# Performance work log

Hardware: AMD Instinct MI355X
Metric: run time of the kernel (lower is better)

The kernel has to match this reference:

```python
import jax, jax.numpy as jnp
import numpy as np

STALK_DIM = 8
K = 5
MARGIN = 0.5
TAU = 0.01
EPS_GAP = 1e-4


def _sheaf_eigenvalues(points, W):
    """Eigenvalues of the sheaf Laplacian L = delta^T delta on a point cloud.

    points: (n, d_in), W: (s, d_in) projection weight (nn.Linear, no bias).
    Faithful to the torch loop, but assembles L directly from its s x s blocks
    (L = delta^T delta expanded per edge) instead of materializing dense delta.
    """
    X = points @ W.T                       # (n, s)
    n, s = X.shape

    # --- fixed topology: KNN on detached coordinates (torch no_grad) ---
    Xd = jax.lax.stop_gradient(X)
    d2 = jnp.sum((Xd[:, None, :] - Xd[None, :, :]) ** 2, axis=-1)  # (n, n)
    nn_idx = jnp.argsort(d2, axis=1)[:, 1:K + 1]                    # (n, K), skip self
    A = jnp.zeros((n, n), dtype=bool).at[jnp.arange(n)[:, None], nn_idx].set(True)
    A = A | A.T                                                     # undirected
    triu = jnp.triu(jnp.ones((n, n), dtype=bool), 1)
    M = (A & triu).astype(points.dtype)    # (n, n) edge mask, canonical i < j

    # --- restriction maps for all ordered pairs i < j (mask selects edges) ---
    d = X[None, :, :] - X[:, None, :]      # d[i, j] = X[j] - X[i], (n, n, s)
    dn = jnp.linalg.norm(d, axis=-1) + 1e-12
    dhat = d / dn[..., None]
    alpha = jnp.minimum(dn, 1.0)
    I_s = jnp.eye(s, dtype=points.dtype)
    # R_ij = I - alpha * dhat dhat^T   (n, n, s, s)
    R = I_s - alpha[..., None, None] * (dhat[..., :, None] * dhat[..., None, :])
    RtR = jnp.einsum('ijab,ijac->ijbc', R, R)

    # --- L = delta^T delta, per edge (i<j): row block [.. I .. -R ..]
    #     contributes  L[i,i]+=I,  L[j,j]+=R^T R,  L[i,j]+=-R,  L[j,i]+=-R^T
    Off = -(M[..., None, None] * R)                     # nonzero only for i<j
    Lb = Off + jnp.swapaxes(jnp.swapaxes(Off, 0, 1), 2, 3)  # add lower blocks
    deg = M.sum(axis=1)                                  # I-blocks at node i
    Djj = jnp.einsum('ij,ijab->jab', M, RtR)             # R^T R blocks at node j
    diag = deg[:, None, None] * I_s + Djj                # (n, s, s)
    Lb = Lb.at[jnp.arange(n), jnp.arange(n)].add(diag)
    L = Lb.transpose(0, 2, 1, 3).reshape(n * s, n * s)
    L = 0.5 * (L + L.T)

    eigs = jnp.linalg.eigvalsh(L)          # ascending, (n*s,)
    return jnp.clip(eigs, 0.0)


def _spectral_gap(eigs):
    gates = jax.nn.sigmoid((eigs - EPS_GAP) / TAU)
    return jnp.sum(eigs * gates) / (jnp.sum(gates) + 1e-12)


def setup_inputs() -> dict:
    key = jax.random.key(0)
    kq, kp, kn, kw = jax.random.split(key, 4)
    n_q, n_pn, d_in = 256, 256, 768
    q_emb = jax.random.normal(kq, (n_q, d_in), dtype=jnp.float32)
    pos_emb = jax.random.normal(kp, (n_pn, d_in), dtype=jnp.float32)
    neg_emb = jax.random.normal(kn, (n_pn, d_in), dtype=jnp.float32)
    # orthogonal init for the projection, as in nn.init.orthogonal_
    G = jax.random.normal(kw, (d_in, STALK_DIM), dtype=jnp.float32)
    Q, _ = jnp.linalg.qr(G)                # (d_in, s) with orthonormal columns
    W = Q.T                                # (s, d_in)
    return {"q_emb": q_emb, "pos_emb": pos_emb, "neg_emb": neg_emb, "W": W}


def reference(q_emb, pos_emb, neg_emb, W):
    pos_cloud = jnp.concatenate([q_emb, pos_emb], axis=0)
    neg_cloud = jnp.concatenate([q_emb, neg_emb], axis=0)
    gap_pos = _spectral_gap(_sheaf_eigenvalues(pos_cloud, W))
    gap_neg = _spectral_gap(_sheaf_eigenvalues(neg_cloud, W))
    triplet = jax.nn.relu(gap_pos - gap_neg + MARGIN)
    return triplet + 0.1 * gap_pos
```

## Files before the change

### kernel.cpp

```cpp
#include <hip/hip_runtime.h>
#include <math.h>

#define NLS    4096
#define NNODE  512
#define SDIM   8
#define KNN_K  5
#define MAXNBR 128
#define DIN    768
#define NB     32
#define GMEGA  448

#define AGLD(p)    __hip_atomic_load((p), __ATOMIC_RELAXED, __HIP_MEMORY_SCOPE_AGENT)
#define AGST(p, v) __hip_atomic_store((p), (v), __ATOMIC_RELAXED, __HIP_MEMORY_SCOPE_AGENT)

struct Ptrs {
  float* X;
  int*   nn;
  int*   nbr;
  int*   cnt;
  float* y;
  float* acol;
  float* vtw;
  float* xn2;
  float* darr;
  float* ebuf;
  float* e2;
  float* bounds;
  float* eigs;
  float* Vt;
  float* Wt;
  float* c1;
  float* c2;
  int*   barmem;
  float* A0;
  float* A1;
};

__device__ __forceinline__ float* matA(const Ptrs& p, int cloud) {
  return cloud == 0 ? p.A0 : p.A1;
}

__device__ __forceinline__ void tbar(int* bm, int act, int bid, int& gen,
                                     int& leafbase, int& rootbase, bool fence) {
  __syncthreads();
  if (threadIdx.x == 0) {
    gen += 1;
    int perleaf = act >> 5;
    if (fence) __threadfence();
    else       __builtin_amdgcn_s_waitcnt(0);
    int* leaf = bm + ((bid & 31) << 4);
    int old = __hip_atomic_fetch_add(leaf, 1, __ATOMIC_RELAXED, __HIP_MEMORY_SCOPE_AGENT);
    if (old == leafbase + perleaf - 1) {
      int ro = __hip_atomic_fetch_add(bm + 512, 1, __ATOMIC_RELAXED, __HIP_MEMORY_SCOPE_AGENT);
      if (ro == rootbase + 31) AGST(bm + 768, gen);
    }
    leafbase += perleaf;
    rootbase += 32;
    while (AGLD(bm + 768) < gen) __builtin_amdgcn_s_sleep(16);
    if (fence) __threadfence();
  }
  __syncthreads();
}

__global__ void zero_kernel(float* ptr, long n) {
  long i = (long)blockIdx.x * 256 + threadIdx.x;
  if (i < n) ptr[i] = 0.f;
}

__global__ void proj_kernel(Ptrs p, const float* q, const float* pe,
                            const float* ne, const float* W) {
  int idx = blockIdx.x * 256 + threadIdx.x;
  if (idx >= 2 * NNODE * SDIM) return;
  int cloud = idx >> 12;
  int rem   = idx & 4095;
  int node  = rem >> 3, t = rem & 7;
  const float* src = (node < 256) ? (q + (size_t)node * DIN)
                                  : ((cloud == 0 ? pe : ne) + (size_t)(node - 256) * DIN);
  const float* wr = W + (size_t)t * DIN;
  float acc = 0.f;
  for (int i = 0; i < DIN; ++i) acc += src[i] * wr[i];
  p.X[(cloud * NNODE + node) * SDIM + t] = acc;
}

__global__ void knn_kernel(Ptrs p) {
  int i = blockIdx.x, cloud = blockIdx.z;
  int lane = threadIdx.x;
  __shared__ float d2s[NNODE];
  const float* X = p.X + cloud * NNODE * SDIM;
  float xi[SDIM];
  for (int t = 0; t < SDIM; ++t) xi[t] = X[i * SDIM + t];
  for (int j = lane; j < NNODE; j += 64) {
    float s = 0.f;
    for (int t = 0; t < SDIM; ++t) { float d = xi[t] - X[j * SDIM + t]; s += d * d; }
    d2s[j] = (j == i) ? 3.4e38f : s;
  }
  __syncthreads();
  for (int r = 0; r < KNN_K; ++r) {
    float bv = 3.39e38f; int bi = NNODE;
    for (int j = lane; j < NNODE; j += 64) {
      float val = d2s[j];
      if (val < bv || (val == bv && j < bi)) { bv = val; bi = j; }
    }
    for (int o = 32; o > 0; o >>= 1) {
      float ov = __shfl_down(bv, o); int oi = __shfl_down(bi, o);
      if (ov < bv || (ov == bv && oi < bi)) { bv = ov; bi = oi; }
    }
    if (lane == 0) {
      p.nn[(cloud * NNODE + i) * KNN_K + r] = bi;
      d2s[bi] = 3.4e38f;
    }
    __syncthreads();
  }
}

__global__ void adj_kernel(Ptrs p) {
  int idx = blockIdx.x * 256 + threadIdx.x;
  if (idx >= 2 * NNODE) return;
  int cloud = idx >> 9, i = idx & 511;
  const int* nn = p.nn + cloud * NNODE * KNN_K;
  int c = 0;
  for (int j = 0; j < NNODE; ++j) {
    if (j == i) continue;
    bool e = false;
    for (int r = 0; r < KNN_K; ++r)
      if (nn[i * KNN_K + r] == j || nn[j * KNN_K + r] == i) e = true;
    if (e) { if (c < MAXNBR) p.nbr[(cloud * NNODE + i) * MAXNBR + c] = j; ++c; }
  }
  p.cnt[cloud * NNODE + i] = (c > MAXNBR ? MAXNBR : c);
}

__global__ void assemble_kernel(Ptrs p, int cloud0) {
  int i = blockIdx.x;
  int cloud = cloud0 + blockIdx.z;
  float* A = matA(p, cloud);
  const float* X = p.X + cloud * NNODE * SDIM;
  const int* nbr = p.nbr + (cloud * NNODE + i) * MAXNBR;
  int cnt = p.cnt[cloud * NNODE + i];
  int tid = threadIdx.x;

  for (int idx = tid; idx < SDIM * NLS; idx += 256) {
    int t = idx >> 12;
    int c = idx & 4095;
    A[(size_t)(i * SDIM + t) * NLS + c] = 0.f;
  }
  __shared__ float diag[64];
  __shared__ float xi[SDIM];
  if (tid < SDIM) xi[tid] = X[i * SDIM + tid];
  if (tid < 64)   diag[tid] = 0.f;
  __syncthreads();

  for (int s = 0; s < cnt; ++s) {
    int j = nbr[s];
    float d[SDIM], ss = 0.f;
    for (int t = 0; t < SDIM; ++t) { d[t] = X[j * SDIM + t] - xi[t]; ss += d[t] * d[t]; }
    float dn = sqrtf(ss) + 1e-12f;
    float alpha = dn < 1.f ? dn : 1.f;
    float inv = 1.f / dn;
    if (tid < 64) {
      int t = tid >> 3, t2 = tid & 7;
      float ut = d[t] * inv, ut2 = d[t2] * inv;
      A[(size_t)(i * SDIM + t) * NLS + j * SDIM + t2] =
          alpha * ut * ut2 - (t == t2 ? 1.f : 0.f);
      if (j < i) {
        float beta = 2.f * alpha - alpha * alpha;
        diag[tid] += beta * ut * ut2;
      }
    }
  }
  __syncthreads();
  if (tid < 64) {
    int t = tid >> 3, t2 = tid & 7;
    A[(size_t)(i * SDIM + t) * NLS + i * SDIM + t2] =
        (t == t2 ? (float)cnt : 0.f) - diag[tid];
  }
}

__global__ __launch_bounds__(256, 4) void mega_kernel(Ptrs p, int cloud0) {
  const int cloud = cloud0 + blockIdx.z;
  const int bid = blockIdx.x;
  float* A  = matA(p, cloud);
  float* Vt = p.Vt + (size_t)cloud * NB * NLS;
  float* Wt = p.Wt + (size_t)cloud * NB * NLS;
  float* yv = p.y + (size_t)cloud * NLS;
  float* acol = p.acol + (size_t)cloud * NLS;
  float* c1g = p.c1 + (size_t)cloud * NLS * NB;
  float* c2g = p.c2 + (size_t)cloud * NLS * NB;
  float* xn2g = p.xn2 + (size_t)cloud * NLS;
  int* bm = p.barmem + (size_t)cloud * 2048;
  int gen = 0, leafbase = 0, rootbase = 0;
  const int tid = threadIdx.x, lane = tid & 63, wv = tid >> 6;

  __shared__ __align__(16) union {
    float v[NLS + 4];
    struct { float Vr[NB][64], Wr[NB][64], Vc[NB][64], Wc[NB][64]; } t;
  } sh;
  __shared__ float c1w[4][NB], c2w[4][NB];
  __shared__ float c1s[NB], c2s[NB], vks[NB], wks[NB];
  __shared__ float red4[4];

  for (int k0 = 0; k0 + NB <= NLS - 64; k0 += NB) {
    int act = (NLS - k0) >> 3;
    act = (act + 31) & ~31;
    if (act < 64)    act = 64;
    if (act > GMEGA) act = GMEGA;
    if (bid >= act) return;

    for (int jj = 0; jj < NB; ++jj) {
      const int k = k0 + jj, s = k + 1, m = NLS - s;
      const int vbase = s & ~3, vn = NLS - vbase;

      float tau, scale;
      if (jj == 0) {
        const float* src = A + (size_t)k * NLS;
        float xp = 0.f;
        for (int i = tid; i < vn; i += 256) {
          int c = vbase + i;
          float a = (c < s) ? 0.f : AGLD((float*)&src[c]);
          sh.v[i] = a;
          if (c > s) xp += a * a;
        }
        for (int o = 32; o > 0; o >>= 1) xp += __shfl_down(xp, o);
        if (lane == 0) red4[wv] = xp;
        __syncthreads();
        float xnorm2 = red4[0] + red4[1] + red4[2] + red4[3];
        float alpha = sh.v[s - vbase];
        float beta;
        if (xnorm2 > 0.f) {
          beta  = -copysignf(sqrtf(alpha * alpha + xnorm2), alpha);
          tau   = (beta - alpha) / beta;
          scale = 1.f / (alpha - beta);
        } else { beta = alpha; tau = 0.f; scale = 0.f; }
        if (bid == 0 && tid == 0) {
          p.darr[cloud * NLS + k] = AGLD((float*)&src[k]);
          p.ebuf[cloud * NLS + k] = beta;
        }
        __syncthreads();
        for (int i = tid; i < vn; i += 256) {
          int c = vbase + i;
          sh.v[i] = (c == s) ? 1.f : ((c < s) ? 0.f : sh.v[i] * scale);
        }
        __syncthreads();
      } else {
        float xnorm2 = AGLD(&xn2g[k]);
        float alpha  = AGLD(&acol[s]);
        float beta;
        if (xnorm2 > 0.f) {
          beta  = -copysignf(sqrtf(alpha * alpha + xnorm2), alpha);
          tau   = (beta - alpha) / beta;
          scale = 1.f / (alpha - beta);
        } else { beta = alpha; tau = 0.f; scale = 0.f; }
        if (bid == 0 && tid == 0) {
          p.darr[cloud * NLS + k] = AGLD(&acol[k]);
          p.ebuf[cloud * NLS + k] = beta;
        }
        for (int i = tid; i < vn; i += 256) {
          int c = vbase + i;
          float a = (c < s) ? 0.f : AGLD(&acol[c]);
          sh.v[i] = (c == s) ? 1.f : a * scale;
        }
        __syncthreads();
      }

      const int nwav = act << 2;
      int B = (m + nwav - 1) / nwav;
      B = (B + 1) & ~1;
      const int r0 = s + ((bid << 2) + wv) * B;
      int r1 = r0 + B; if (r1 > NLS) r1 = NLS;
      float vtyloc = 0.f, c1p = 0.f, c2p = 0.f;
      const int l2i = lane - 32;
      for (int r = r0; r < r1; r += 2) {
        const bool two = (r + 1 < r1);
        const float* Ar0 = A + (size_t)r * NLS;
        const float* Ar1 = two ? (Ar0 + NLS) : Ar0;
        float acc0 = 0.f, acc1 = 0.f;
        #pragma unroll 4
        for (int c = vbase + (lane << 2); c < NLS; c += 256) {
          const float4 v4 = *(const float4*)(&sh.v[c - vbase]);
          const float4 a0 = *(const float4*)(Ar0 + c);
          const float4 a1 = *(const float4*)(Ar1 + c);
          acc0 += a0.x * v4.x + a0.y * v4.y + a0.z * v4.z + a0.w * v4.w;
          acc1 += a1.x * v4.x + a1.y * v4.y + a1.z * v4.z + a1.w * v4.w;
        }
        for (int o = 32; o > 0; o >>= 1) {
          acc0 += __shfl_down(acc0, o);
          acc1 += __shfl_down(acc1, o);
        }
        float vr0 = sh.v[r - vbase];
        float vr1 = two ? sh.v[r + 1 - vbase] : 0.f;
        if (lane == 0) {
          AGST(&yv[r], acc0);
          if (two) AGST(&yv[r + 1], acc1);
          vtyloc += vr0 * acc0 + vr1 * acc1;
        }
        if (lane < jj) {
          const float* Wl = Wt + (size_t)lane * NLS;
          c1p += Wl[r] * vr0 + (two ? Wl[r + 1] * vr1 : 0.f);
        }
        if (l2i >= 0 && l2i < jj) {
          const float* Vl = Vt + (size_t)l2i * NLS;
          c2p += Vl[r] * vr0 + (two ? Vl[r + 1] * vr1 : 0.f);
        }
      }
      if (lane == 0) red4[wv] = vtyloc;
      if (lane < 32)      c1w[wv][lane] = (lane < jj) ? c1p : 0.f;
      else                c2w[wv][l2i]  = (l2i  < jj) ? c2p : 0.f;
      __syncthreads();
      if (tid == 0) {
        float t = red4[0] + red4[1] + red4[2] + red4[3];
        if (t != 0.f) atomicAdd(&p.vtw[cloud * NLS + k], t);
      }
      if (tid < jj) {
        float t = c1w[0][tid] + c1w[1][tid] + c1w[2][tid] + c1w[3][tid];
        if (t != 0.f) atomicAdd(&c1g[(size_t)k * NB + tid], t);
      } else if (tid >= 64 && tid < 64 + jj) {
        int j2 = tid - 64;
        float t = c2w[0][j2] + c2w[1][j2] + c2w[2][j2] + c2w[3][j2];
        if (t != 0.f) atomicAdd(&c2g[(size_t)k * NB + j2], t);
      }

      tbar(bm, act, bid, gen, leafbase, rootbase, false);

      if (tid < jj) {
        c1s[tid] = AGLD(&c1g[(size_t)k * NB + tid]);
        c2s[tid] = AGLD(&c2g[(size_t)k * NB + tid]);
        vks[tid] = Vt[(size_t)tid * NLS + s];
        wks[tid] = Wt[(size_t)tid * NLS + s];
      }
      __syncthreads();
      float vty = AGLD(&p.vtw[cloud * NLS + k]);
      float dotc = 0.f, corrs = 0.f;
      for (int j2 = 0; j2 < jj; ++j2) {
        dotc  += c1s[j2] * c2s[j2];
        corrs += vks[j2] * c1s[j2] + wks[j2] * c2s[j2];
      }
      float s2v = tau * (vty - 2.f * dotc);
      float ys  = AGLD(&yv[s]);
      float wfirst = tau * ys - tau * corrs - 0.5f * tau * s2v;
      bool havenext = (jj < NB - 1);
      const float* Arow = A + (size_t)s * NLS;
      float xpart = 0.f;
      for (int r = s + (bid << 8) + tid; r < NLS; r += (act << 8)) {
        float vr = sh.v[r - vbase];
        float yr = AGLD(&yv[r]);
        float corr = 0.f, ac2 = 0.f;
        for (int j2 = 0; j2 < jj; ++j2) {
          float vj = Vt[(size_t)j2 * NLS + r];
          float wj = Wt[(size_t)j2 * NLS + r];
          corr += vj * c1s[j2] + wj * c2s[j2];
          ac2  += vj * wks[j2] + wj * vks[j2];
        }
        float wr = tau * yr - tau * corr - 0.5f * tau * s2v * vr;
        AGST(&Vt[(size_t)jj * NLS + r], vr);
        AGST(&Wt[(size_t)jj * NLS + r], wr);
        if (havenext) {
          float ac = Arow[r] - ac2 - (vr * wfirst + wr);
          AGST(&acol[r], ac);
          if (r >= s + 2) xpart += ac * ac;
        }
      }
      if (havenext) {
        for (int o = 32; o > 0; o >>= 1) xpart += __shfl_down(xpart, o);
        if (lane == 0) red4[wv] = xpart;
        __syncthreads();
        if (tid == 0) {
          float t = red4[0] + red4[1] + red4[2] + red4[3];
          if (t != 0.f) atomicAdd(&xn2g[k + 1], t);
        }
      }

      tbar(bm, act, bid, gen, leafbase, rootbase, false);
    }

    {
      const int base2 = k0 + NB;
      const int nt = (NLS - base2 + 63) >> 6;
      const int ntt = nt * nt;
      for (int it = bid; it < ntt; it += act) {
        int by = it / nt, bx = it - by * nt;
        int r0t = base2 + (by << 6), c0t = base2 + (bx << 6);
        __syncthreads();
        for (int idx = tid; idx < NB * 64; idx += 256) {
          int j4 = idx >> 6, i = idx & 63;
          int r = r0t + i, c = c0t + i;
          sh.t.Vr[j4][i] = (r < NLS) ? Vt[(size_t)j4 * NLS + r] : 0.f;
          sh.t.Wr[j4][i] = (r < NLS) ? Wt[(size_t)j4 * NLS + r] : 0.f;
          sh.t.Vc[j4][i] = (c < NLS) ? Vt[(size_t)j4 * NLS + c] : 0.f;
          sh.t.Wc[j4][i] = (c < NLS) ? Wt[(size_t)j4 * NLS + c] : 0.f;
        }
        __syncthreads();
        int ty = tid >> 4, tx = tid & 15;
        float acc[4][4] = {{0.f}};
        for (int j4 = 0; j4 < NB; ++j4) {
          float vr[4], wr[4], vc[4], wc[4];
          for (int a = 0; a < 4; ++a) {
            vr[a] = sh.t.Vr[j4][ty * 4 + a]; wr[a] = sh.t.Wr[j4][ty * 4 + a];
            vc[a] = sh.t.Vc[j4][tx * 4 + a]; wc[a] = sh.t.Wc[j4][tx * 4 + a];
          }
          for (int a = 0; a < 4; ++a)
            for (int b = 0; b < 4; ++b)
              acc[a][b] += vr[a] * wc[b] + wr[a] * vc[b];
        }
        for (int a = 0; a < 4; ++a) {
          int r = r0t + ty * 4 + a;
          int c = c0t + tx * 4;
          if (r < NLS && c < NLS) {
            float4* pa = (float4*)&A[(size_t)r * NLS + c];
            float4 old = *pa;
            old.x -= acc[a][0]; old.y -= acc[a][1];
            old.z -= acc[a][2]; old.w -= acc[a][3];
            *pa = old;
          }
        }
      }
      tbar(bm, act, bid, gen, leafbase, rootbase, true);
    }
  }
}

__global__ void ktrail_kernel(Ptrs p, int cloud0) {
  int cloud = cloud0 + blockIdx.z;
  float* A = matA(p, cloud);
  const int base = NLS - 64;
  int lane = threadIdx.x;
  __shared__ float B[64][65];
  __shared__ float vv[64], ww[64];
  for (int r = 0; r < 64; ++r)
    B[r][lane] = A[(size_t)(base + r) * NLS + base + lane];
  __syncthreads();
  for (int kl = 0; kl <= 61; ++kl) {
    float val = (lane >= kl + 2) ? B[kl][lane] : 0.f;
    float part = val * val;
    for (int o = 32; o > 0; o >>= 1) part += __shfl_xor(part, o);
    float xnorm2 = part;
    float alpha = B[kl][kl + 1];
    float beta, tau, scale;
    if (xnorm2 > 0.f) {
      beta  = -copysignf(sqrtf(alpha * alpha + xnorm2), alpha);
      tau   = (beta - alpha) / beta;
      scale = 1.f / (alpha - beta);
    } else { beta = alpha; tau = 0.f; scale = 0.f; }
    if (lane == 0) {
      p.darr[cloud * NLS + base + kl] = B[kl][kl];
      p.ebuf[cloud * NLS + base + kl] = beta;
    }
    vv[lane] = (lane == kl + 1) ? 1.f : ((lane >= kl + 2) ? B[kl][lane] * scale : 0.f);
    __syncthreads();
    float yv = 0.f;
    if (lane >= kl + 1)
      for (int c = kl + 1; c < 64; ++c) yv += B[lane][c] * vv[c];
    float vy = (lane >= kl + 1) ? vv[lane] * yv : 0.f;
    for (int o = 32; o > 0; o >>= 1) vy += __shfl_xor(vy, o);
    float w = tau * yv - 0.5f * tau * (tau * vy) * vv[lane];
    ww[lane] = (lane >= kl + 1) ? w : 0.f;
    __syncthreads();
    if (lane >= kl + 1) {
      float vr = vv[lane], wr = ww[lane];
      for (int c = kl + 1; c < 64; ++c)
        B[lane][c] -= vr * ww[c] + wr * vv[c];
    }
    __syncthreads();
  }
  if (lane == 0) {
    p.darr[cloud * NLS + base + 62] = B[62][62];
    p.darr[cloud * NLS + base + 63] = B[63][63];
    p.ebuf[cloud * NLS + base + 62] = B[63][62];
    p.ebuf[cloud * NLS + base + 63] = 0.f;
  }
}

__global__ void gather_kernel(Ptrs p, int cloud0) {
  int cloud = cloud0 + blockIdx.z;
  const int n = NLS;
  int tid = threadIdx.x;
  const float* d = p.darr + cloud * NLS;
  float* e2 = p.e2 + cloud * NLS;
  __shared__ float elds[NLS];
  for (int i = tid; i < n; i += 1024) {
    float e = (i < n - 1) ? p.ebuf[cloud * NLS + i] : 0.f;
    e2[i]   = e * e;
    elds[i] = fabsf(e);
  }
  __syncthreads();
  float lo = 3.4e38f, hi = -3.4e38f;
  for (int i = tid; i < n; i += 1024) {
    float rad = elds[i] + (i > 0 ? elds[i - 1] : 0.f);
    lo = fminf(lo, d[i] - rad);
    hi = fmaxf(hi, d[i] + rad);
  }
  __shared__ float rl[16], rh[16];
  int lane = tid & 63, wv = tid >> 6;
  for (int o = 32; o > 0; o >>= 1) {
    lo = fminf(lo, __shfl_down(lo, o));
    hi = fmaxf(hi, __shfl_down(hi, o));
  }
  if (lane == 0) { rl[wv] = lo; rh[wv] = hi; }
  __syncthreads();
  if (tid == 0) {
    for (int t = 1; t < 16; ++t) { lo = fminf(lo, rl[t]); hi = fmaxf(hi, rh[t]); }
    p.bounds[cloud * 2 + 0] = lo - 0.5f;
    p.bounds[cloud * 2 + 1] = hi + 0.5f;
  }
}

__global__ void bisect_kernel(Ptrs p, int cloud0) {
  int cloud = cloud0 + blockIdx.z;
  int idx = blockIdx.x * 256 + threadIdx.x;
  const float* d  = p.darr + cloud * NLS;
  const float* e2 = p.e2   + cloud * NLS;
  float lo = p.bounds[cloud * 2 + 0];
  float hi = p.bounds[cloud * 2 + 1];
  const float pivmin = 1e-28f;
  for (int it = 0; it < 34; ++it) {
    float mid = 0.5f * (lo + hi);
    int cnt = 0;
    float qq = d[0] - mid;
    if (fabsf(qq) < pivmin) qq = -pivmin;
    cnt += (qq < 0.f);
    for (int i = 1; i < NLS; ++i) {
      qq = d[i] - mid - e2[i - 1] / qq;
      if (fabsf(qq) < pivmin) qq = -pivmin;
      cnt += (qq < 0.f);
    }
    if (cnt > idx) hi = mid; else lo = mid;
  }
  float ev = 0.5f * (lo + hi);
  p.eigs[cloud * NLS + idx] = ev > 0.f ? ev : 0.f;
}

__global__ void final_kernel(Ptrs p, float* out) {
  __shared__ float lds[64];
  int tid = threadIdx.x;
  for (int cloud = 0; cloud < 2; ++cloud) {
    float num = 0.f, den = 0.f;
    for (int i = tid; i < NLS; i += 256) {
      float lam = p.eigs[cloud * NLS + i];
      float g = 1.f / (1.f + expf(-(lam - 1e-4f) * 100.f));
      num += lam * g;
      den += g;
    }
    for (int o = 32; o > 0; o >>= 1) {
      num += __shfl_down(num, o);
      den += __shfl_down(den, o);
    }
    if ((tid & 63) == 0) { lds[(tid >> 6) * 2] = num; lds[(tid >> 6) * 2 + 1] = den; }
    __syncthreads();
    if (tid == 0) {
      float N = lds[0] + lds[2] + lds[4] + lds[6];
      float D = lds[1] + lds[3] + lds[5] + lds[7];
      lds[32 + cloud] = N / (D + 1e-12f);
    }
    __syncthreads();
  }
  if (tid == 0) {
    float gp = lds[32], gn = lds[33];
    float trip = gp - gn + 0.5f;
    if (trip < 0.f) trip = 0.f;
    out[0] = trip + 0.1f * gp;
  }
}

extern "C" void kernel_launch(void* const* d_in, const int* in_sizes, int n_in,
                              void* d_out, int out_size, void* d_ws, size_t ws_size,
                              hipStream_t stream) {
  const float* q  = (const float*)d_in[0];
  const float* pe = (const float*)d_in[1];
  const float* ne = (const float*)d_in[2];
  const float* W  = (const float*)d_in[3];

  char* base = (char*)d_ws;
  size_t off = 0;
  auto alloc = [&](size_t nbytes) -> void* {
    off = (off + 255) & ~(size_t)255;
    void* r = base + off;
    off += nbytes;
    return r;
  };

  Ptrs p;
  p.X      = (float*)alloc(sizeof(float) * 2 * NNODE * SDIM);
  p.nn     = (int*)  alloc(sizeof(int)   * 2 * NNODE * KNN_K);
  p.nbr    = (int*)  alloc(sizeof(int)   * 2 * NNODE * MAXNBR);
  p.cnt    = (int*)  alloc(sizeof(int)   * 2 * NNODE);
  p.y      = (float*)alloc(sizeof(float) * 2 * NLS);
  p.acol   = (float*)alloc(sizeof(float) * 2 * NLS);
  p.darr   = (float*)alloc(sizeof(float) * 2 * NLS);
  p.ebuf   = (float*)alloc(sizeof(float) * 2 * NLS);
  p.e2     = (float*)alloc(sizeof(float) * 2 * NLS);
  p.bounds = (float*)alloc(sizeof(float) * 4);
  p.eigs   = (float*)alloc(sizeof(float) * 2 * NLS);
  p.Vt     = (float*)alloc(sizeof(float) * 2 * NB * NLS);
  p.Wt     = (float*)alloc(sizeof(float) * 2 * NB * NLS);

  size_t zstart = (off + 255) & ~(size_t)255;
  p.vtw    = (float*)alloc(sizeof(float) * 2 * NLS);
  p.xn2    = (float*)alloc(sizeof(float) * 2 * NLS);
  p.c1     = (float*)alloc(sizeof(float) * 2 * NLS * NB);
  p.c2     = (float*)alloc(sizeof(float) * 2 * NLS * NB);
  p.barmem = (int*)  alloc(sizeof(int)   * 2 * 2048);
  size_t zend = off;
  long zcount = (long)((zend - zstart) / 4);

  const size_t Abytes = (size_t)NLS * NLS * sizeof(float);
  p.A0 = (float*)alloc(Abytes);
  size_t offA1 = (off + 255) & ~(size_t)255;
  bool batched = (offA1 + Abytes) <= ws_size;
  p.A1 = batched ? (float*)alloc(Abytes) : p.A0;

  zero_kernel<<<dim3((int)((zcount + 255) / 256)), 256, 0, stream>>>((float*)(base + zstart), zcount);
  proj_kernel<<<dim3(32), 256, 0, stream>>>(p, q, pe, ne, W);
  knn_kernel<<<dim3(NNODE, 1, 2), 64, 0, stream>>>(p);
  adj_kernel<<<dim3(4), 256, 0, stream>>>(p);

  auto run_cloud = [&](int cloud0, int z) {
    assemble_kernel<<<dim3(NNODE, 1, z), 256, 0, stream>>>(p, cloud0);
    mega_kernel<<<dim3(GMEGA, 1, z), 256, 0, stream>>>(p, cloud0);
    ktrail_kernel<<<dim3(1, 1, z), 64, 0, stream>>>(p, cloud0);
    gather_kernel<<<dim3(1, 1, z), 1024, 0, stream>>>(p, cloud0);
    bisect_kernel<<<dim3(NLS / 256, 1, z), 256, 0, stream>>>(p, cloud0);
  };

  if (batched) {
    run_cloud(0, 2);
  } else {
    run_cloud(0, 1);
    run_cloud(1, 1);
  }

  final_kernel<<<dim3(1), 256, 0, stream>>>(p, (float*)d_out);
}
```

Baseline: 106.3 ms.

## Exploit symmetry in Householder matvec with lower-triangular tiles

The per-column symmetric matrix-vector product in the blocked tridiagonalization is restructured. Each block now loads a 64x64 lower-triangle tile of A into shared memory and computes both the row and the transposed contribution, so roughly half of the trailing matrix is read. Partial results are accumulated into a double-buffered y vector with atomics, and the next buffer is zeroed during the update phase. The c1/c2 correction dot products become separate work items instead of being folded into the row loop. In exchange the kernel performs many more global atomic adds, needs extra shared memory and adds more syncthreads per tile.

```diff
diff --git a/kernel.cpp b/kernel.cpp
--- a/kernel.cpp
+++ b/kernel.cpp
@@ -181,7 +181,6 @@
   float* A  = matA(p, cloud);
   float* Vt = p.Vt + (size_t)cloud * NB * NLS;
   float* Wt = p.Wt + (size_t)cloud * NB * NLS;
-  float* yv = p.y + (size_t)cloud * NLS;
   float* acol = p.acol + (size_t)cloud * NLS;
   float* c1g = p.c1 + (size_t)cloud * NLS * NB;
   float* c2g = p.c2 + (size_t)cloud * NLS * NB;
@@ -191,10 +190,14 @@
   const int tid = threadIdx.x, lane = tid & 63, wv = tid >> 6;
 
   __shared__ __align__(16) union {
-    float v[NLS + 4];
+    struct {
+      float v[NLS + 4];
+      float tile[64][65];
+      float rpw[4][64];
+      float cpw[4][64];
+    } p1;
     struct { float Vr[NB][64], Wr[NB][64], Vc[NB][64], Wc[NB][64]; } t;
   } sh;
-  __shared__ float c1w[4][NB], c2w[4][NB];
   __shared__ float c1s[NB], c2s[NB], vks[NB], wks[NB];
   __shared__ float red4[4];
 
@@ -206,8 +209,11 @@
     if (bid >= act) return;
 
     for (int jj = 0; jj < NB; ++jj) {
-      const int k = k0 + jj, s = k + 1, m = NLS - s;
-      const int vbase = s & ~3, vn = NLS - vbase;
+      const int k = k0 + jj, s = k + 1;
+      const int vbase = s & ~63;
+      const int vn = NLS - vbase;
+      float* yv    = p.y + ((size_t)cloud * 2 + (k & 1)) * NLS;
+      float* ynext = p.y + ((size_t)cloud * 2 + ((k + 1) & 1)) * NLS;
 
       float tau, scale;
       if (jj == 0) {
@@ -216,14 +222,14 @@
         for (int i = tid; i < vn; i += 256) {
           int c = vbase + i;
           float a = (c < s) ? 0.f : AGLD((float*)&src[c]);
-          sh.v[i] = a;
+          sh.p1.v[i] = a;
           if (c > s) xp += a * a;
         }
         for (int o = 32; o > 0; o >>= 1) xp += __shfl_down(xp, o);
         if (lane == 0) red4[wv] = xp;
         __syncthreads();
         float xnorm2 = red4[0] + red4[1] + red4[2] + red4[3];
-        float alpha = sh.v[s - vbase];
+        float alpha = sh.p1.v[s - vbase];
         float beta;
         if (xnorm2 > 0.f) {
           beta  = -copysignf(sqrtf(alpha * alpha + xnorm2), alpha);
@@ -237,7 +243,7 @@
         __syncthreads();
         for (int i = tid; i < vn; i += 256) {
           int c = vbase + i;
-          sh.v[i] = (c == s) ? 1.f : ((c < s) ? 0.f : sh.v[i] * scale);
+          sh.p1.v[i] = (c == s) ? 1.f : ((c < s) ? 0.f : sh.p1.v[i] * scale);
         }
         __syncthreads();
       } else {
@@ -256,66 +262,89 @@
         for (int i = tid; i < vn; i += 256) {
           int c = vbase + i;
           float a = (c < s) ? 0.f : AGLD(&acol[c]);
-          sh.v[i] = (c == s) ? 1.f : a * scale;
-        }
-        __syncthreads();
-      }
-
-      const int nwav = act << 2;
-      int B = (m + nwav - 1) / nwav;
-      B = (B + 1) & ~1;
-      const int r0 = s + ((bid << 2) + wv) * B;
-      int r1 = r0 + B; if (r1 > NLS) r1 = NLS;
-      float vtyloc = 0.f, c1p = 0.f, c2p = 0.f;
-      const int l2i = lane - 32;
-      for (int r = r0; r < r1; r += 2) {
-        const bool two = (r + 1 < r1);
-        const float* Ar0 = A + (size_t)r * NLS;
-        const float* Ar1 = two ? (Ar0 + NLS) : Ar0;
-        float acc0 = 0.f, acc1 = 0.f;
-        #pragma unroll 4
-        for (int c = vbase + (lane << 2); c < NLS; c += 256) {
-          const float4 v4 = *(const float4*)(&sh.v[c - vbase]);
-          const float4 a0 = *(const float4*)(Ar0 + c);
-          const float4 a1 = *(const float4*)(Ar1 + c);
-          acc0 += a0.x * v4.x + a0.y * v4.y + a0.z * v4.z + a0.w * v4.w;
-          acc1 += a1.x * v4.x + a1.y * v4.y + a1.z * v4.z + a1.w * v4.w;
-        }
-        for (int o = 32; o > 0; o >>= 1) {
-          acc0 += __shfl_down(acc0, o);
-          acc1 += __shfl_down(acc1, o);
-        }
-        float vr0 = sh.v[r - vbase];
-        float vr1 = two ? sh.v[r + 1 - vbase] : 0.f;
-        if (lane == 0) {
-          AGST(&yv[r], acc0);
-          if (two) AGST(&yv[r + 1], acc1);
-          vtyloc += vr0 * acc0 + vr1 * acc1;
-        }
-        if (lane < jj) {
-          const float* Wl = Wt + (size_t)lane * NLS;
-          c1p += Wl[r] * vr0 + (two ? Wl[r + 1] * vr1 : 0.f);
-        }
-        if (l2i >= 0 && l2i < jj) {
-          const float* Vl = Vt + (size_t)l2i * NLS;
-          c2p += Vl[r] * vr0 + (two ? Vl[r + 1] * vr1 : 0.f);
-        }
-      }
+          sh.p1.v[i] = (c == s) ? 1.f : ((c < s) ? 0.f : a * scale);
+        }
+        __syncthreads();
+      }
+
+      const int nt = vn >> 6;
+      const int T = (nt * (nt + 1)) >> 1;
+      const int nwork = T + jj;
+      float vtyloc = 0.f;
+      for (int item = bid; item < nwork; item += act) {
+        __syncthreads();
+        if (item < T) {
+          int I = (int)((sqrtf(8.f * (float)item + 1.f) - 1.f) * 0.5f);
+          while (((I + 1) * (I + 2)) / 2 <= item) ++I;
+          while ((I * (I + 1)) / 2 > item) --I;
+          int J = item - (I * (I + 1)) / 2;
+          const int R0 = vbase + (I << 6), C0 = vbase + (J << 6);
+          const bool dg = (I == J);
+          for (int idx = tid; idx < 1024; idx += 256) {
+            int i = idx >> 4, q = idx & 15;
+            const float4 val = *(const float4*)(A + (size_t)(R0 + i) * NLS + C0 + (q << 2));
+            float* dst = &sh.p1.tile[i][q << 2];
+            dst[0] = val.x; dst[1] = val.y; dst[2] = val.z; dst[3] = val.w;
+          }
+          __syncthreads();
+          float rp = 0.f, cp = 0.f;
+          {
+            const float* vrow = &sh.p1.v[C0 - vbase];
+            const float* vcol = &sh.p1.v[R0 - vbase];
+            const int j0 = wv << 4;
+            if (dg) {
+              for (int j = j0; j < j0 + 16; ++j)
+                rp += sh.p1.tile[lane][j] * vrow[j];
+            } else {
+              for (int j = j0; j < j0 + 16; ++j) {
+                rp += sh.p1.tile[lane][j] * vrow[j];
+                cp += sh.p1.tile[j][lane] * vcol[j];
+              }
+            }
+          }
+          sh.p1.rpw[wv][lane] = rp;
+          sh.p1.cpw[wv][lane] = cp;
+          __syncthreads();
+          if (wv == 0) {
+            float rsum = sh.p1.rpw[0][lane] + sh.p1.rpw[1][lane]
+                       + sh.p1.rpw[2][lane] + sh.p1.rpw[3][lane];
+            if (rsum != 0.f) atomicAdd(&yv[R0 + lane], rsum);
+            vtyloc += rsum * sh.p1.v[R0 + lane - vbase];
+          } else if (wv == 1 && !dg) {
+            float csum = sh.p1.cpw[0][lane] + sh.p1.cpw[1][lane]
+                       + sh.p1.cpw[2][lane] + sh.p1.cpw[3][lane];
+            if (csum != 0.f) atomicAdd(&yv[C0 + lane], csum);
+            vtyloc += csum * sh.p1.v[C0 + lane - vbase];
+          }
+        } else {
+          int j2 = item - T;
+          float s1 = 0.f, s2 = 0.f;
+          for (int r = s + tid; r < NLS; r += 256) {
+            float v = sh.p1.v[r - vbase];
+            s1 += Wt[(size_t)j2 * NLS + r] * v;
+            s2 += Vt[(size_t)j2 * NLS + r] * v;
+          }
+          for (int o = 32; o > 0; o >>= 1) {
+            s1 += __shfl_down(s1, o);
+            s2 += __shfl_down(s2, o);
+          }
+          if (lane == 0) { sh.p1.rpw[wv][0] = s1; sh.p1.rpw[wv][1] = s2; }
+          __syncthreads();
+          if (tid == 0) {
+            AGST(&c1g[(size_t)k * NB + j2],
+                 sh.p1.rpw[0][0] + sh.p1.rpw[1][0] + sh.p1.rpw[2][0] + sh.p1.rpw[3][0]);
+            AGST(&c2g[(size_t)k * NB + j2],
+                 sh.p1.rpw[0][1] + sh.p1.rpw[1][1] + sh.p1.rpw[2][1] + sh.p1.rpw[3][1]);
+          }
+        }
+      }
+      for (int o = 32; o > 0; o >>= 1) vtyloc += __shfl_down(vtyloc, o);
+      __syncthreads();
       if (lane == 0) red4[wv] = vtyloc;
-      if (lane < 32)      c1w[wv][lane] = (lane < jj) ? c1p : 0.f;
-      else                c2w[wv][l2i]  = (l2i  < jj) ? c2p : 0.f;
       __syncthreads();
       if (tid == 0) {
         float t = red4[0] + red4[1] + red4[2] + red4[3];
         if (t != 0.f) atomicAdd(&p.vtw[cloud * NLS + k], t);
-      }
-      if (tid < jj) {
-        float t = c1w[0][tid] + c1w[1][tid] + c1w[2][tid] + c1w[3][tid];
-        if (t != 0.f) atomicAdd(&c1g[(size_t)k * NB + tid], t);
-      } else if (tid >= 64 && tid < 64 + jj) {
-        int j2 = tid - 64;
-        float t = c2w[0][j2] + c2w[1][j2] + c2w[2][j2] + c2w[3][j2];
-        if (t != 0.f) atomicAdd(&c2g[(size_t)k * NB + j2], t);
       }
 
       tbar(bm, act, bid, gen, leafbase, rootbase, false);
@@ -340,7 +369,7 @@
       const float* Arow = A + (size_t)s * NLS;
       float xpart = 0.f;
       for (int r = s + (bid << 8) + tid; r < NLS; r += (act << 8)) {
-        float vr = sh.v[r - vbase];
+        float vr = sh.p1.v[r - vbase];
         float yr = AGLD(&yv[r]);
         float corr = 0.f, ac2 = 0.f;
         for (int j2 = 0; j2 < jj; ++j2) {
@@ -352,6 +381,7 @@
         float wr = tau * yr - tau * corr - 0.5f * tau * s2v * vr;
         AGST(&Vt[(size_t)jj * NLS + r], vr);
         AGST(&Wt[(size_t)jj * NLS + r], wr);
+        AGST(&ynext[r], 0.f);
         if (havenext) {
           float ac = Arow[r] - ac2 - (vr * wfirst + wr);
           AGST(&acol[r], ac);
@@ -373,10 +403,10 @@
 
     {
       const int base2 = k0 + NB;
-      const int nt = (NLS - base2 + 63) >> 6;
-      const int ntt = nt * nt;
+      const int nt2 = (NLS - base2 + 63) >> 6;
+      const int ntt = nt2 * nt2;
       for (int it = bid; it < ntt; it += act) {
-        int by = it / nt, bx = it - by * nt;
+        int by = it / nt2, bx = it - by * nt2;
         int r0t = base2 + (by << 6), c0t = base2 + (bx << 6);
         __syncthreads();
         for (int idx = tid; idx < NB * 64; idx += 256) {
@@ -581,7 +611,6 @@
   p.nn     = (int*)  alloc(sizeof(int)   * 2 * NNODE * KNN_K);
   p.nbr    = (int*)  alloc(sizeof(int)   * 2 * NNODE * MAXNBR);
   p.cnt    = (int*)  alloc(sizeof(int)   * 2 * NNODE);
-  p.y      = (float*)alloc(sizeof(float) * 2 * NLS);
   p.acol   = (float*)alloc(sizeof(float) * 2 * NLS);
   p.darr   = (float*)alloc(sizeof(float) * 2 * NLS);
   p.ebuf   = (float*)alloc(sizeof(float) * 2 * NLS);
@@ -592,6 +621,7 @@
   p.Wt     = (float*)alloc(sizeof(float) * 2 * NB * NLS);
 
   size_t zstart = (off + 255) & ~(size_t)255;
+  p.y      = (float*)alloc(sizeof(float) * 2 * 2 * NLS);
   p.vtw    = (float*)alloc(sizeof(float) * 2 * NLS);
   p.xn2    = (float*)alloc(sizeof(float) * 2 * NLS);
   p.c1     = (float*)alloc(sizeof(float) * 2 * NLS * NB);
```

Result: faster. 102.6 ms (-3.4%).
